# Kernel tuning notes

Hardware: AMD Instinct MI355X
Metric: run time of the kernel (lower is better)

## Reference

```python
import jax, jax.numpy as jnp
import numpy as np

MATRIX_DIM = 128
FEAT = MATRIX_DIM * (MATRIX_DIM + 1) // 2  # 8256, triu incl. diagonal
HID = FEAT // 5                            # 1651
BATCH = 4096


def setup_inputs() -> dict:
    key = jax.random.key(0)
    k0, k1, k2, k3, k4 = jax.random.split(key, 5)
    stdv1 = 1.0 / FEAT / 2.0
    stdv2 = 1.0 / HID / 2.0
    return {
        "sim_matrices": jax.random.normal(k0, (BATCH, MATRIX_DIM, MATRIX_DIM), dtype=jnp.float32),
        "W1": jax.random.uniform(k1, (HID, FEAT), minval=-stdv1, maxval=stdv1, dtype=jnp.float32),
        "b1": jax.random.uniform(k2, (HID,), minval=-stdv1, maxval=stdv1, dtype=jnp.float32),
        "W2": jax.random.uniform(k3, (1, HID), minval=-stdv2, maxval=stdv2, dtype=jnp.float32),
        "b2": jax.random.uniform(k4, (1,), minval=-stdv2, maxval=stdv2, dtype=jnp.float32),
    }


def reference(sim_matrices, W1, b1, W2, b2):
    # flatten: take upper-triangular (incl. diag) entries -> [B, FEAT]
    iu0, iu1 = np.triu_indices(sim_matrices.shape[1])
    x = sim_matrices[:, iu0, iu1]
    # Linear_block 1 (ideal crossbar VMM = W x + b) + ReLU
    h = jax.nn.relu(jnp.einsum("bf,hf->bh", x, W1) + b1)
    # Linear_block 2 + Sigmoid -> [B, 1]
    return jax.nn.sigmoid(jnp.einsum("bh,oh->bo", h, W2) + b2)
```

## Files before the change

kernel.cpp:

```cpp
#include <hip/hip_runtime.h>
#include <hip/hip_bf16.h>
#include <math.h>

#define MDIM  128
#define FEAT  8256
#define HID   1651
#define HIDP  1664
#define BATCH 4096
#define BK    64
#define KT_TOTAL 129
#define NZ    2
#define KT_PER 64

using f32x4  = __attribute__((ext_vector_type(4))) float;
using bf16x8 = __attribute__((ext_vector_type(8))) __bf16;

__device__ __forceinline__ void gload_lds16(const void* g, void* l) {
    __builtin_amdgcn_global_load_lds(
        (const __attribute__((address_space(1))) void*)g,
        (__attribute__((address_space(3))) void*)l,
        16, 0, 0);
}

__device__ __forceinline__ int row_off(int i) { return (i * (257 - i)) >> 1; }

__global__ void __launch_bounds__(256)
pack_x_kernel(const float* __restrict__ sim,
              __hip_bfloat16* __restrict__ X) {
    __shared__ __hip_bfloat16 s[MDIM * MDIM];
    const int b = blockIdx.x;
    const int t = threadIdx.x;

    const f32x4* src = (const f32x4*)(sim + ((long long)b << 14));
#pragma unroll
    for (int it = 0; it < 16; ++it) {
        const int idx = it * 256 + t;
        const f32x4 v = src[idx];
        __hip_bfloat16* d = &s[idx * 4];
        d[0] = __float2bfloat16(v[0]);
        d[1] = __float2bfloat16(v[1]);
        d[2] = __float2bfloat16(v[2]);
        d[3] = __float2bfloat16(v[3]);
    }
    __syncthreads();

    __hip_bfloat16* dst = X + (long long)b * FEAT;
#pragma unroll
    for (int it = 0; it < 5; ++it) {
        const int w = it * 256 + t;
        if (w < FEAT / 8) {
            const int f0 = w * 8;
            int i = (int)((257.0f - sqrtf(66049.0f - 8.0f * (float)f0)) * 0.5f);
            i = i < 0 ? 0 : (i > 127 ? 127 : i);
            while (i < 127 && row_off(i + 1) <= f0) ++i;
            while (i > 0 && row_off(i) > f0) --i;
            int j = i + (f0 - row_off(i));
            __align__(16) __hip_bfloat16 tmp[8];
#pragma unroll
            for (int e = 0; e < 8; ++e) {
                if (j > 127) { ++i; j = i; }
                tmp[e] = s[i * MDIM + j];
                ++j;
            }
            *(bf16x8*)(dst + f0) = *(const bf16x8*)tmp;
        }
    }
}

__global__ void __launch_bounds__(256)
conv_w1_kernel(const float* __restrict__ W1,
               __hip_bfloat16* __restrict__ W1p) {
    const int w = blockIdx.x * 256 + threadIdx.x;
    if (w >= FEAT / 8) return;
    const int n  = blockIdx.y;
    const int f0 = w * 8;
    __align__(16) __hip_bfloat16 tmp[8];
    if (n < HID) {
        const float* src = W1 + (long long)n * FEAT + f0;
        const f32x4 a = *(const f32x4*)src;
        const f32x4 c = *(const f32x4*)(src + 4);
#pragma unroll
        for (int e = 0; e < 4; ++e) {
            tmp[e]     = __float2bfloat16(a[e]);
            tmp[e + 4] = __float2bfloat16(c[e]);
        }
    } else {
#pragma unroll
        for (int e = 0; e < 8; ++e) tmp[e] = __float2bfloat16(0.0f);
    }
    *(bf16x8*)(W1p + (long long)n * FEAT + f0) = *(const bf16x8*)tmp;
}

__global__ void __launch_bounds__(256, 2)
gemm_split_kernel(const __hip_bfloat16* __restrict__ X,
                  const __hip_bfloat16* __restrict__ W1p,
                  __hip_bfloat16* __restrict__ Cz) {
    __shared__ __align__(16) __hip_bfloat16 lds_a[128 * BK];
    __shared__ __align__(16) __hip_bfloat16 lds_b[128 * BK];

    const int t    = threadIdx.x;
    const int wave = t >> 6;
    const int lane = t & 63;
    const int bm   = blockIdx.x;
    const int bn   = blockIdx.y;
    const int z    = blockIdx.z;
    const int wm   = wave >> 1;
    const int wn   = wave & 1;
    const int lr   = lane & 15;
    const int lq   = lane >> 4;

    f32x4 acc[4][4];
#pragma unroll
    for (int i = 0; i < 4; ++i)
#pragma unroll
        for (int j = 0; j < 4; ++j)
            acc[i][j] = (f32x4){0.f, 0.f, 0.f, 0.f};

    const int kt0 = z * KT_PER;
    const int nkt = (z == NZ - 1) ? (KT_TOTAL - KT_PER * (NZ - 1)) : KT_PER;

    const int swc = (t & 7) ^ ((t >> 3) & 7);
    const __hip_bfloat16* gA =
        X + (long long)(bm * 128 + (t >> 3)) * FEAT + swc * 8 + kt0 * BK;
    const __hip_bfloat16* gB =
        W1p + (long long)(bn * 128 + (t >> 3)) * FEAT + swc * 8 + kt0 * BK;
    __hip_bfloat16* lA = lds_a + wave * 512;
    __hip_bfloat16* lB = lds_b + wave * 512;

    for (int kt = 0; kt < nkt; ++kt) {
#pragma unroll
        for (int s = 0; s < 4; ++s) {
            gload_lds16(gA + (long long)s * 32 * FEAT, lA + s * 2048);
            gload_lds16(gB + (long long)s * 32 * FEAT, lB + s * 2048);
        }
        gA += BK;
        gB += BK;
        __syncthreads();

#pragma unroll
        for (int ks = 0; ks < 2; ++ks) {
            bf16x8 af[4], bfr[4];
#pragma unroll
            for (int i = 0; i < 4; ++i) {
                const int ra = wm * 64 + i * 16 + lr;
                const int rb = wn * 64 + i * 16 + lr;
                const int kc = ks * 4 + lq;
                af[i]  = *(const bf16x8*)&lds_a[(ra * 8 + (kc ^ (lr & 7))) * 8];
                bfr[i] = *(const bf16x8*)&lds_b[(rb * 8 + (kc ^ (lr & 7))) * 8];
            }
#pragma unroll
            for (int i = 0; i < 4; ++i)
#pragma unroll
                for (int j = 0; j < 4; ++j)
                    acc[i][j] = __builtin_amdgcn_mfma_f32_16x16x32_bf16(
                        af[i], bfr[j], acc[i][j], 0, 0, 0);
        }
        __syncthreads();
    }

    __hip_bfloat16* cz = Cz + ((long long)z * BATCH + bm * 128) * HIDP
                            + bn * 128 + wn * 64;
#pragma unroll
    for (int i = 0; i < 4; ++i)
#pragma unroll
        for (int r = 0; r < 4; ++r) {
            const int ml = wm * 64 + i * 16 + lq * 4 + r;
#pragma unroll
            for (int j = 0; j < 4; ++j)
                cz[(long long)ml * HIDP + j * 16 + lr] =
                    __float2bfloat16(acc[i][j][r]);
        }
}

__global__ void __launch_bounds__(256)
epilogue_kernel(const __hip_bfloat16* __restrict__ Cz,
                const float* __restrict__ b1,
                const float* __restrict__ W2,
                const float* __restrict__ b2,
                float* __restrict__ out) {
    const int b = blockIdx.x;
    const int t = threadIdx.x;
    float sum = 0.0f;
    const bf16x8* r0 = (const bf16x8*)(Cz + (long long)b * HIDP);
    const bf16x8* r1 = (const bf16x8*)(Cz + ((long long)BATCH + b) * HIDP);
    if (t < HIDP / 8) {
        const bf16x8 a = r0[t];
        const bf16x8 c = r1[t];
#pragma unroll
        for (int e = 0; e < 8; ++e) {
            const int n = t * 8 + e;
            if (n < HID) {
                const float v = (float)a[e] + (float)c[e] + b1[n];
                sum += fmaxf(v, 0.0f) * W2[n];
            }
        }
    }
    sum += __shfl_xor(sum, 1);
    sum += __shfl_xor(sum, 2);
    sum += __shfl_xor(sum, 4);
    sum += __shfl_xor(sum, 8);
    sum += __shfl_xor(sum, 16);
    sum += __shfl_xor(sum, 32);
    __shared__ float wsum[4];
    if ((t & 63) == 0) wsum[t >> 6] = sum;
    __syncthreads();
    if (t == 0) {
        const float s = wsum[0] + wsum[1] + wsum[2] + wsum[3];
        out[b] = 1.0f / (1.0f + expf(-(s + b2[0])));
    }
}

extern "C" void kernel_launch(void* const* d_in, const int* in_sizes, int n_in,
                              void* d_out, int out_size, void* d_ws, size_t ws_size,
                              hipStream_t stream) {
    const float* sim = (const float*)d_in[0];
    const float* W1  = (const float*)d_in[1];
    const float* b1  = (const float*)d_in[2];
    const float* W2  = (const float*)d_in[3];
    const float* b2  = (const float*)d_in[4];
    float* out = (float*)d_out;

    char* ws = (char*)d_ws;
    const long long X_OFF   = 0;
    const long long W1P_OFF = 67633152LL;
    const long long CZ_OFF  = W1P_OFF + 27475968LL;
    __hip_bfloat16* X   = (__hip_bfloat16*)(ws + X_OFF);
    __hip_bfloat16* W1p = (__hip_bfloat16*)(ws + W1P_OFF);
    __hip_bfloat16* Cz  = (__hip_bfloat16*)(ws + CZ_OFF);

    pack_x_kernel<<<BATCH, 256, 0, stream>>>(sim, X);
    {
        dim3 grid((FEAT / 8 + 255) / 256, HIDP);
        conv_w1_kernel<<<grid, 256, 0, stream>>>(W1, W1p);
    }
    {
        dim3 grid(BATCH / 128, HIDP / 128, NZ);
        gemm_split_kernel<<<grid, 256, 0, stream>>>(X, W1p, Cz);
    }
    epilogue_kernel<<<BATCH, 256, 0, stream>>>(Cz, b1, W2, b2, out);
}
```

Before: 577.5 us.

## Switch GEMM operands to FP8 with scaled W1 and FP8 MFMA

Quantizes the packed activations and W1 to FP8 (e4m3), scaling W1 by 8192 to keep it in range, and runs the GEMM with the 16x16x32 FP8 MFMA instruction. LDS tiles and global-to-LDS loads are re-laid-out for byte-sized elements with a new swizzle, and occupancy is raised to 4 blocks per CU. The pack kernel now reads from global directly instead of staging the matrix in LDS. The aim is to halve operand bandwidth and LDS footprint and to use the higher-throughput FP8 path. The cost is lower numerical precision, which may matter for the tolerance check.

```diff
diff --git a/kernel.cpp b/kernel.cpp
--- a/kernel.cpp
+++ b/kernel.cpp
@@ -11,9 +11,12 @@
 #define KT_TOTAL 129
 #define NZ    2
 #define KT_PER 64
+#define W1SCALE 8192.0f
+#define W1INV   (1.0f / 8192.0f)
 
 using f32x4  = __attribute__((ext_vector_type(4))) float;
 using bf16x8 = __attribute__((ext_vector_type(8))) __bf16;
+typedef long long i64;
 
 __device__ __forceinline__ void gload_lds16(const void* g, void* l) {
     __builtin_amdgcn_global_load_lds(
@@ -24,27 +27,20 @@
 
 __device__ __forceinline__ int row_off(int i) { return (i * (257 - i)) >> 1; }
 
+__device__ __forceinline__ void pack8_fp8(const float* f, int* o) {
+    int lo = __builtin_amdgcn_cvt_pk_fp8_f32(f[0], f[1], 0, false);
+    lo     = __builtin_amdgcn_cvt_pk_fp8_f32(f[2], f[3], lo, true);
+    int hi = __builtin_amdgcn_cvt_pk_fp8_f32(f[4], f[5], 0, false);
+    hi     = __builtin_amdgcn_cvt_pk_fp8_f32(f[6], f[7], hi, true);
+    o[0] = lo; o[1] = hi;
+}
+
 __global__ void __launch_bounds__(256)
-pack_x_kernel(const float* __restrict__ sim,
-              __hip_bfloat16* __restrict__ X) {
-    __shared__ __hip_bfloat16 s[MDIM * MDIM];
+pack_x_kernel(const float* __restrict__ sim, char* __restrict__ X) {
     const int b = blockIdx.x;
     const int t = threadIdx.x;
-
-    const f32x4* src = (const f32x4*)(sim + ((long long)b << 14));
-#pragma unroll
-    for (int it = 0; it < 16; ++it) {
-        const int idx = it * 256 + t;
-        const f32x4 v = src[idx];
-        __hip_bfloat16* d = &s[idx * 4];
-        d[0] = __float2bfloat16(v[0]);
-        d[1] = __float2bfloat16(v[1]);
-        d[2] = __float2bfloat16(v[2]);
-        d[3] = __float2bfloat16(v[3]);
-    }
-    __syncthreads();
-
-    __hip_bfloat16* dst = X + (long long)b * FEAT;
+    const float* srow = sim + ((long long)b << 14);
+    char* dst = X + (long long)b * FEAT;
 #pragma unroll
     for (int it = 0; it < 5; ++it) {
         const int w = it * 256 + t;
@@ -55,48 +51,50 @@
             while (i < 127 && row_off(i + 1) <= f0) ++i;
             while (i > 0 && row_off(i) > f0) --i;
             int j = i + (f0 - row_off(i));
-            __align__(16) __hip_bfloat16 tmp[8];
+            float v[8];
 #pragma unroll
             for (int e = 0; e < 8; ++e) {
                 if (j > 127) { ++i; j = i; }
-                tmp[e] = s[i * MDIM + j];
+                v[e] = srow[i * MDIM + j];
                 ++j;
             }
-            *(bf16x8*)(dst + f0) = *(const bf16x8*)tmp;
+            int o[2];
+            pack8_fp8(v, o);
+            *(int2*)(dst + f0) = make_int2(o[0], o[1]);
         }
     }
 }
 
 __global__ void __launch_bounds__(256)
-conv_w1_kernel(const float* __restrict__ W1,
-               __hip_bfloat16* __restrict__ W1p) {
+conv_w1_kernel(const float* __restrict__ W1, char* __restrict__ W1p) {
     const int w = blockIdx.x * 256 + threadIdx.x;
     if (w >= FEAT / 8) return;
     const int n  = blockIdx.y;
     const int f0 = w * 8;
-    __align__(16) __hip_bfloat16 tmp[8];
+    int o[2];
     if (n < HID) {
         const float* src = W1 + (long long)n * FEAT + f0;
         const f32x4 a = *(const f32x4*)src;
         const f32x4 c = *(const f32x4*)(src + 4);
+        float v[8];
 #pragma unroll
         for (int e = 0; e < 4; ++e) {
-            tmp[e]     = __float2bfloat16(a[e]);
-            tmp[e + 4] = __float2bfloat16(c[e]);
-        }
+            v[e]     = a[e] * W1SCALE;
+            v[e + 4] = c[e] * W1SCALE;
+        }
+        pack8_fp8(v, o);
     } else {
-#pragma unroll
-        for (int e = 0; e < 8; ++e) tmp[e] = __float2bfloat16(0.0f);
-    }
-    *(bf16x8*)(W1p + (long long)n * FEAT + f0) = *(const bf16x8*)tmp;
-}
-
-__global__ void __launch_bounds__(256, 2)
-gemm_split_kernel(const __hip_bfloat16* __restrict__ X,
-                  const __hip_bfloat16* __restrict__ W1p,
+        o[0] = 0; o[1] = 0;
+    }
+    *(int2*)(W1p + (long long)n * FEAT + f0) = make_int2(o[0], o[1]);
+}
+
+__global__ void __launch_bounds__(256, 4)
+gemm_split_kernel(const char* __restrict__ X,
+                  const char* __restrict__ W1p,
                   __hip_bfloat16* __restrict__ Cz) {
-    __shared__ __align__(16) __hip_bfloat16 lds_a[128 * BK];
-    __shared__ __align__(16) __hip_bfloat16 lds_b[128 * BK];
+    __shared__ __align__(16) char lds_a[128 * BK];
+    __shared__ __align__(16) char lds_b[128 * BK];
 
     const int t    = threadIdx.x;
     const int wave = t >> 6;
@@ -119,19 +117,22 @@
     const int kt0 = z * KT_PER;
     const int nkt = (z == NZ - 1) ? (KT_TOTAL - KT_PER * (NZ - 1)) : KT_PER;
 
-    const int swc = (t & 7) ^ ((t >> 3) & 7);
-    const __hip_bfloat16* gA =
-        X + (long long)(bm * 128 + (t >> 3)) * FEAT + swc * 8 + kt0 * BK;
-    const __hip_bfloat16* gB =
-        W1p + (long long)(bn * 128 + (t >> 3)) * FEAT + swc * 8 + kt0 * BK;
-    __hip_bfloat16* lA = lds_a + wave * 512;
-    __hip_bfloat16* lB = lds_b + wave * 512;
+    const int swst = (t & 3) ^ ((t >> 2) & 3) ^ ((t >> 4) & 3);
+    const char* gA = X + (long long)(bm * 128 + (t >> 2)) * FEAT
+                       + kt0 * BK + swst * 16;
+    const char* gB = W1p + (long long)(bn * 128 + (t >> 2)) * FEAT
+                         + kt0 * BK + swst * 16;
+    char* lA = lds_a + wave * 1024;
+    char* lB = lds_b + wave * 1024;
+
+    const int ksw = (lq & 1) * 8;
+    const int cl  = lq >> 1;
 
     for (int kt = 0; kt < nkt; ++kt) {
 #pragma unroll
-        for (int s = 0; s < 4; ++s) {
-            gload_lds16(gA + (long long)s * 32 * FEAT, lA + s * 2048);
-            gload_lds16(gB + (long long)s * 32 * FEAT, lB + s * 2048);
+        for (int s = 0; s < 2; ++s) {
+            gload_lds16(gA + (long long)s * 64 * FEAT, lA + s * 4096);
+            gload_lds16(gB + (long long)s * 64 * FEAT, lB + s * 4096);
         }
         gA += BK;
         gB += BK;
@@ -139,21 +140,24 @@
 
 #pragma unroll
         for (int ks = 0; ks < 2; ++ks) {
-            bf16x8 af[4], bfr[4];
+            i64 av[4], bv[4];
 #pragma unroll
             for (int i = 0; i < 4; ++i) {
                 const int ra = wm * 64 + i * 16 + lr;
                 const int rb = wn * 64 + i * 16 + lr;
-                const int kc = ks * 4 + lq;
-                af[i]  = *(const bf16x8*)&lds_a[(ra * 8 + (kc ^ (lr & 7))) * 8];
-                bfr[i] = *(const bf16x8*)&lds_b[(rb * 8 + (kc ^ (lr & 7))) * 8];
+                const int swa = (ra & 3) ^ ((ra >> 2) & 3);
+                const int swb = (rb & 3) ^ ((rb >> 2) & 3);
+                const int pa = ((ks * 2 + cl) ^ swa);
+                const int pb = ((ks * 2 + cl) ^ swb);
+                av[i] = *(const i64*)(lds_a + ra * 64 + pa * 16 + ksw);
+                bv[i] = *(const i64*)(lds_b + rb * 64 + pb * 16 + ksw);
             }
 #pragma unroll
             for (int i = 0; i < 4; ++i)
 #pragma unroll
                 for (int j = 0; j < 4; ++j)
-                    acc[i][j] = __builtin_amdgcn_mfma_f32_16x16x32_bf16(
-                        af[i], bfr[j], acc[i][j], 0, 0, 0);
+                    acc[i][j] = __builtin_amdgcn_mfma_f32_16x16x32_fp8_fp8(
+                        av[i], bv[j], acc[i][j], 0, 0, 0);
         }
         __syncthreads();
     }
@@ -190,7 +194,7 @@
         for (int e = 0; e < 8; ++e) {
             const int n = t * 8 + e;
             if (n < HID) {
-                const float v = (float)a[e] + (float)c[e] + b1[n];
+                const float v = ((float)a[e] + (float)c[e]) * W1INV + b1[n];
                 sum += fmaxf(v, 0.0f) * W2[n];
             }
         }
@@ -222,20 +226,20 @@
 
     char* ws = (char*)d_ws;
     const long long X_OFF   = 0;
-    const long long W1P_OFF = 67633152LL;
-    const long long CZ_OFF  = W1P_OFF + 27475968LL;
-    __hip_bfloat16* X   = (__hip_bfloat16*)(ws + X_OFF);
-    __hip_bfloat16* W1p = (__hip_bfloat16*)(ws + W1P_OFF);
-    __hip_bfloat16* Cz  = (__hip_bfloat16*)(ws + CZ_OFF);
-
-    pack_x_kernel<<<BATCH, 256, 0, stream>>>(sim, X);
+    const long long W1P_OFF = (long long)BATCH * FEAT;
+    const long long CZ_OFF  = W1P_OFF + (long long)HIDP * FEAT;
+    char*           Xf8  = ws + X_OFF;
+    char*           W1f8 = ws + W1P_OFF;
+    __hip_bfloat16* Cz   = (__hip_bfloat16*)(ws + CZ_OFF);
+
+    pack_x_kernel<<<BATCH, 256, 0, stream>>>(sim, Xf8);
     {
         dim3 grid((FEAT / 8 + 255) / 256, HIDP);
-        conv_w1_kernel<<<grid, 256, 0, stream>>>(W1, W1p);
+        conv_w1_kernel<<<grid, 256, 0, stream>>>(W1, W1f8);
     }
     {
         dim3 grid(BATCH / 128, HIDP / 128, NZ);
-        gemm_split_kernel<<<grid, 256, 0, stream>>>(X, W1p, Cz);
+        gemm_split_kernel<<<grid, 256, 0, stream>>>(Xf8, W1f8, Cz);
     }
     epilogue_kernel<<<BATCH, 256, 0, stream>>>(Cz, b1, W2, b2, out);
 }
```

After: 503.6 us. 1.15x faster.
